# Performance work log

Measured on AMD Instinct MI355X. Metric: run time of the kernel, lower is better.

The kernel has to match this reference:

```python
import jax, jax.numpy as jnp
import numpy as np

MASK_SCORE = -1.0e15
LOG_2PI = float(np.log(2.0 * np.pi))


def setup_inputs() -> dict:
    key = jax.random.key(0)
    k1, k2, k3, k4 = jax.random.split(key, 4)
    B, H, N, T = 32, 256, 512, 2048
    encoder_outputs = jax.random.normal(k1, (B, H, N), dtype=jnp.float32)
    # positive integer-like durations in [1, 7]
    durations = jnp.round(jax.random.uniform(k2, (B, N), minval=1.0, maxval=7.0)).astype(jnp.float32)
    # well-conditioned variances
    vars_ = jax.random.uniform(k3, (B, N), minval=0.5, maxval=2.0, dtype=jnp.float32)
    input_lengths = jax.random.randint(k4, (B,), N // 2, N + 1, dtype=jnp.int32)
    return {"encoder_outputs": encoder_outputs, "durations": durations,
            "vars": vars_, "input_lengths": input_lengths, "T": T}


def reference(encoder_outputs, durations, vars, input_lengths, T):
    # encoder_outputs: [B, H, N] -> [B, N, H]
    x = jnp.swapaxes(encoder_outputs, 1, 2)
    B, N, H = x.shape
    # Gaussian centers: cumsum(d) - d/2  -> [B, N]
    c = jnp.cumsum(durations, axis=1) - 0.5 * durations
    t = jnp.arange(T, dtype=x.dtype)  # [T]
    v = vars[:, :, None]              # [B, N, 1]
    # Gaussian log-density scores: [B, N, T]
    w_t = -0.5 * (LOG_2PI + jnp.log(v) + jnp.square(t[None, None, :] - c[:, :, None]) / v)
    # mask invalid phoneme positions (index >= length) along N
    invalid = jnp.arange(N)[None, :] >= input_lengths[:, None]  # [B, N]
    w_t = jnp.where(invalid[:, :, None], MASK_SCORE, w_t)
    # softmax over phoneme axis N, then weighted sum of encoder states
    w_t = jax.nn.softmax(w_t, axis=1)                 # [B, N, T]
    out = jnp.einsum('bnt,bnh->bth', w_t, x)          # [B, T, H]
    return jnp.swapaxes(out, 1, 2)                    # [B, H, T]
```

## Files before the change

### kernel.cpp

```cpp
#include <hip/hip_runtime.h>
#include <math.h>
#include <stdint.h>

static constexpr int B = 32, H = 256, N = 512, T = 2048;
static constexpr int TTILE = 64;
static constexpr int KC = 64;
static constexpr float kLOG_2PI = 1.8378770664093453f;
static constexpr float kLOG2E   = 1.4426950408889634f;
static constexpr float kNEG_BIG = -3.0e38f;
static constexpr float kRANGE_DELTA = 26.0f;

typedef __attribute__((ext_vector_type(8))) short bf16x8;
typedef __attribute__((ext_vector_type(4))) float f32x4;

static __device__ __forceinline__ short f2bf(float f) {
  unsigned u = __float_as_uint(f);
  unsigned r = (u + 0x7fffu + ((u >> 16) & 1u)) >> 16;
  return (short)r;
}

__global__ void k_prep(const float* __restrict__ dur, const float* __restrict__ vars,
                       const int* __restrict__ lens,
                       float4* __restrict__ psg, float2* __restrict__ bstat) {
  const int b = blockIdx.x;
  const int lane = threadIdx.x;
  const int L = lens[b];
  float running = 0.f;
  float rc[N / 64], ra2[N / 64], rq2[N / 64];
  float a2max = kNEG_BIG, a2min = -kNEG_BIG, q2min = -kNEG_BIG, q2max = kNEG_BIG;
  float dmax = 0.f, clast = 0.f;
#pragma unroll
  for (int i = 0; i < N / 64; ++i) {
    const int n = i * 64 + lane;
    const float d = dur[b * N + n];
    float x = d;
#pragma unroll
    for (int off = 1; off < 64; off <<= 1) {
      float up = __shfl_up(x, off, 64);
      if (lane >= off) x += up;
    }
    const float cc = running + x - 0.5f * d;
    running += __shfl(x, 63, 64);
    const float v = vars[b * N + n];
    const float a2v = -0.5f * (kLOG_2PI + logf(v)) * kLOG2E;
    const float q2v = 0.5f * kLOG2E / v;
    rc[i] = cc; ra2[i] = a2v; rq2[i] = q2v;
    if (n < L) {
      a2max = fmaxf(a2max, a2v); a2min = fminf(a2min, a2v);
      q2min = fminf(q2min, q2v); q2max = fmaxf(q2max, q2v);
      dmax = fmaxf(dmax, d);
      if (n == L - 1) clast = cc;
    }
  }
#pragma unroll
  for (int off = 32; off; off >>= 1) {
    a2max = fmaxf(a2max, __shfl_xor(a2max, off, 64));
    a2min = fminf(a2min, __shfl_xor(a2min, off, 64));
    q2min = fminf(q2min, __shfl_xor(q2min, off, 64));
    q2max = fmaxf(q2max, __shfl_xor(q2max, off, 64));
    dmax  = fmaxf(dmax,  __shfl_xor(dmax,  off, 64));
    clast = fmaxf(clast, __shfl_xor(clast, off, 64));
  }
  const float dnb = 0.5f * dmax;
  const float m_lower = a2min - q2max * dnb * dnb;
  const float thr = m_lower - kRANGE_DELTA;
#pragma unroll
  for (int i = 0; i < N / 64; ++i) {
    const int n = i * 64 + lane;
    const float rr = sqrtf(fmaxf(ra2[i] - thr, 0.f) / rq2[i]);
    psg[(size_t)b * N + n] = make_float4(rc[i], ra2[i], rq2[i], rr);
  }
  if (lane == 0) bstat[b] = make_float2(a2max, clast);
}

__global__ __launch_bounds__(256) void k_fused(
    const float* __restrict__ enc, const float4* __restrict__ psg,
    const int* __restrict__ lens, const float2* __restrict__ bstat,
    float* __restrict__ out) {
  __shared__ float4 ps[N];
  __shared__ float m_lds[TTILE];
  __shared__ int range_sh[2];

  const int b = blockIdx.y;
  const int t0 = blockIdx.x * TTILE;
  const int tid = threadIdx.x;
  const int lane = tid & 63;
  const int wave = tid >> 6;
  const int L = lens[b];
  const float2 bs = bstat[b];
  const float* encb = enc + (size_t)b * H * N;
  const float4* psb = psg + (size_t)b * N;

  const int l15 = lane & 15;
  const int lhi = lane >> 4;
  const int arow0 = wave * 64 + l15;

  const bool tile_near = ((float)(t0 + TTILE - 1) <= bs.y);
  int nlo, nhi;
  float mt[4];

  if (tile_near) {
    const float tmin = (float)t0, tmax = (float)(t0 + TTILE - 1);
    int lo = N, hi = -1;
#pragma unroll
    for (int rr = 0; rr < 8; ++rr) {
      const int n = rr * 64 + lane;
      const float4 p4 = psb[n];
      if (n < L && (p4.x - p4.w) <= tmax && (p4.x + p4.w) >= tmin) {
        lo = min(lo, n); hi = max(hi, n);
      }
    }
#pragma unroll
    for (int off = 32; off; off >>= 1) {
      lo = min(lo, __shfl_xor(lo, off, 64));
      hi = max(hi, __shfl_xor(hi, off, 64));
    }
    nlo = lo; nhi = hi;
#pragma unroll
    for (int tt = 0; tt < 4; ++tt) mt[tt] = bs.x;
  } else {
    if (tid == 0) { range_sh[0] = N; range_sh[1] = -1; }
    for (int i = tid; i < N; i += 256) ps[i] = psb[i];
    __syncthreads();
    const int tl = tid >> 2, j = tid & 3;
    const float tf = (float)(t0 + tl);
    const int iL = (L + 3) >> 2;
    float mA = kNEG_BIG, mB = kNEG_BIG;
    int i1 = 0;
    for (; i1 + 1 < iL; i1 += 2) {
      const int n1 = i1 * 4 + j, n2 = n1 + 4;
      const float4 p1 = ps[n1];
      const float tc1 = tf - p1.x;
      const float w1 = fmaf(-p1.z, tc1 * tc1, p1.y);
      mA = fmaxf(mA, (n1 < L) ? w1 : kNEG_BIG);
      const float4 p2 = ps[n2];
      const float tc2 = tf - p2.x;
      const float w2 = fmaf(-p2.z, tc2 * tc2, p2.y);
      mB = fmaxf(mB, (n2 < L) ? w2 : kNEG_BIG);
    }
    if (i1 < iL) {
      const int n1 = i1 * 4 + j;
      const float4 p1 = ps[n1];
      const float tc1 = tf - p1.x;
      const float w1 = fmaf(-p1.z, tc1 * tc1, p1.y);
      mA = fmaxf(mA, (n1 < L) ? w1 : kNEG_BIG);
    }
    float m = fmaxf(mA, mB);
    m = fmaxf(m, __shfl_xor(m, 1, 64));
    m = fmaxf(m, __shfl_xor(m, 2, 64));
    if (j == 0) m_lds[tl] = m;

    const float thr = m - kRANGE_DELTA;
    int lo = N, hi = -1;
    for (int i2 = 0; i2 < iL; ++i2) {
      const int n = i2 * 4 + j;
      const float4 p4 = ps[n];
      const float tc = tf - p4.x;
      const float ww = fmaf(-p4.z, tc * tc, p4.y);
      if (n < L && ww >= thr) { lo = min(lo, n); hi = max(hi, n); }
    }
#pragma unroll
    for (int off = 32; off; off >>= 1) {
      lo = min(lo, __shfl_xor(lo, off, 64));
      hi = max(hi, __shfl_xor(hi, off, 64));
    }
    if (lane == 0) { atomicMin(&range_sh[0], lo); atomicMax(&range_sh[1], hi); }
    __syncthreads();
    nlo = range_sh[0]; nhi = range_sh[1];
#pragma unroll
    for (int tt = 0; tt < 4; ++tt) mt[tt] = m_lds[tt * 16 + l15];
  }

  if (nhi < 0) { nlo = 0; nhi = L - 1; }
  nlo = max(0, min(nlo, N - 1)); nhi = max(nlo, min(nhi, N - 1));

  f32x4 acc[4][4];
#pragma unroll
  for (int mf = 0; mf < 4; ++mf)
#pragma unroll
    for (int tt = 0; tt < 4; ++tt) acc[mf][tt] = (f32x4){0.f, 0.f, 0.f, 0.f};
  float psum[4] = {0.f, 0.f, 0.f, 0.f};

  int wb = nlo & ~3;
  while (true) {
    const int wbc = min(wb, N - KC);
    const int wlo = max(wb, nlo);
#pragma unroll
    for (int kk = 0; kk < KC; kk += 32) {
      const int colk = wbc + kk;
      if (colk > nhi || colk + 31 < wlo) continue;
      const int col = colk + lhi * 8;
      float4 pq[8];
#pragma unroll
      for (int jj = 0; jj < 8; ++jj) pq[jj] = psb[col + jj];
      bf16x8 aF[4];
#pragma unroll
      for (int mf = 0; mf < 4; ++mf) {
        const float* src = encb + (size_t)(arow0 + mf * 16) * N + col;
        const float4 v0 = *(const float4*)(src);
        const float4 v1 = *(const float4*)(src + 4);
        aF[mf][0] = f2bf(v0.x); aF[mf][1] = f2bf(v0.y);
        aF[mf][2] = f2bf(v0.z); aF[mf][3] = f2bf(v0.w);
        aF[mf][4] = f2bf(v1.x); aF[mf][5] = f2bf(v1.y);
        aF[mf][6] = f2bf(v1.z); aF[mf][7] = f2bf(v1.w);
      }
#pragma unroll
      for (int tt = 0; tt < 4; ++tt) {
        const float tft = (float)(t0 + tt * 16 + l15);
        const float mtt = mt[tt];
        bf16x8 bF;
        float psv = 0.f;
#pragma unroll
        for (int jj = 0; jj < 8; ++jj) {
          const int n = col + jj;
          const float tc = tft - pq[jj].x;
          const float w2v = fmaf(-pq[jj].z, tc * tc, pq[jj].y);
          const float pv = (n >= wlo && n <= nhi) ? exp2f(w2v - mtt) : 0.f;
          psv += pv;
          bF[jj] = f2bf(pv);
        }
        psum[tt] += psv;
#pragma unroll
        for (int mf = 0; mf < 4; ++mf)
          acc[mf][tt] = __builtin_amdgcn_mfma_f32_16x16x32_bf16(aF[mf], bF, acc[mf][tt], 0, 0, 0);
      }
    }
    if (wbc + KC > nhi) break;
    wb = wbc + KC;
  }

#pragma unroll
  for (int tt = 0; tt < 4; ++tt) {
    float s = psum[tt];
    s += __shfl_xor(s, 16, 64);
    s += __shfl_xor(s, 32, 64);
    const float is = 1.0f / s;
    const int t = tt * 16 + l15;
#pragma unroll
    for (int mf = 0; mf < 4; ++mf) {
      const int h = wave * 64 + mf * 16 + lhi * 4;
#pragma unroll
      for (int r = 0; r < 4; ++r) {
        out[((size_t)(b * H + h + r)) * T + t0 + t] = acc[mf][tt][r] * is;
      }
    }
  }
}

extern "C" void kernel_launch(void* const* d_in, const int* in_sizes, int n_in,
                              void* d_out, int out_size, void* d_ws, size_t ws_size,
                              hipStream_t stream) {
  const float* enc  = (const float*)d_in[0];
  const float* dur  = (const float*)d_in[1];
  const float* vars = (const float*)d_in[2];
  const int*   lens = (const int*)d_in[3];
  float* out = (float*)d_out;

  char* ws = (char*)d_ws;
  float4* psg   = (float4*)ws;
  float2* bstat = (float2*)(psg + B * N);

  k_prep<<<B, 64, 0, stream>>>(dur, vars, lens, psg, bstat);
  k_fused<<<dim3(T / TTILE, B), 256, 0, stream>>>(enc, psg, lens, bstat, out);
}
```

Measured before the change: 41.38 us.

## Split near/far tiles into separate kernels and bound far-tile scan range

Splits the fused kernel into a near-tile kernel, which uses a constant per-batch max, and a far-tile kernel, which narrows its max and range scan to phonemes whose centres could still matter. The far path no longer stages the parameters in shared memory and starts scanning from a lower bound computed in prep. It also halves the K chunk to 32 and switches to the library bf16 conversion. The intent is less divergent code per kernel and less scanning work for far tiles, at the cost of one extra launch and many early-exiting blocks.

```diff
diff --git a/kernel.cpp b/kernel.cpp
--- a/kernel.cpp
+++ b/kernel.cpp
@@ -1,10 +1,11 @@
 #include <hip/hip_runtime.h>
+#include <hip/hip_bf16.h>
 #include <math.h>
 #include <stdint.h>
 
 static constexpr int B = 32, H = 256, N = 512, T = 2048;
 static constexpr int TTILE = 64;
-static constexpr int KC = 64;
+static constexpr int KC = 32;
 static constexpr float kLOG_2PI = 1.8378770664093453f;
 static constexpr float kLOG2E   = 1.4426950408889634f;
 static constexpr float kNEG_BIG = -3.0e38f;
@@ -14,14 +15,13 @@
 typedef __attribute__((ext_vector_type(4))) float f32x4;
 
 static __device__ __forceinline__ short f2bf(float f) {
-  unsigned u = __float_as_uint(f);
-  unsigned r = (u + 0x7fffu + ((u >> 16) & 1u)) >> 16;
-  return (short)r;
+  __hip_bfloat16 h = __float2bfloat16(f);
+  return *reinterpret_cast<short*>(&h);
 }
 
 __global__ void k_prep(const float* __restrict__ dur, const float* __restrict__ vars,
                        const int* __restrict__ lens,
-                       float4* __restrict__ psg, float2* __restrict__ bstat) {
+                       float4* __restrict__ psg, float4* __restrict__ bstat) {
   const int b = blockIdx.x;
   const int lane = threadIdx.x;
   const int L = lens[b];
@@ -70,109 +70,49 @@
     const float rr = sqrtf(fmaxf(ra2[i] - thr, 0.f) / rq2[i]);
     psg[(size_t)b * N + n] = make_float4(rc[i], ra2[i], rq2[i], rr);
   }
-  if (lane == 0) bstat[b] = make_float2(a2max, clast);
-}
-
-__global__ __launch_bounds__(256) void k_fused(
+  if (lane == 0) {
+    bstat[b] = make_float4(a2max, clast,
+                           sqrtf(q2max / q2min) - 1.0f,
+                           sqrtf(fmaxf(a2max - a2min + kRANGE_DELTA + 1.0f, 0.f) / q2min));
+  }
+}
+
+__global__ __launch_bounds__(256) void k_near(
     const float* __restrict__ enc, const float4* __restrict__ psg,
-    const int* __restrict__ lens, const float2* __restrict__ bstat,
+    const int* __restrict__ lens, const float4* __restrict__ bstat,
     float* __restrict__ out) {
-  __shared__ float4 ps[N];
-  __shared__ float m_lds[TTILE];
-  __shared__ int range_sh[2];
-
   const int b = blockIdx.y;
   const int t0 = blockIdx.x * TTILE;
+  const float4 bs = bstat[b];
+  if ((float)(t0 + TTILE - 1) > bs.y) return;
   const int tid = threadIdx.x;
   const int lane = tid & 63;
   const int wave = tid >> 6;
   const int L = lens[b];
-  const float2 bs = bstat[b];
   const float* encb = enc + (size_t)b * H * N;
   const float4* psb = psg + (size_t)b * N;
-
-  const int l15 = lane & 15;
-  const int lhi = lane >> 4;
+  const int l15 = lane & 15, lhi = lane >> 4;
   const int arow0 = wave * 64 + l15;
 
-  const bool tile_near = ((float)(t0 + TTILE - 1) <= bs.y);
-  int nlo, nhi;
-  float mt[4];
-
-  if (tile_near) {
-    const float tmin = (float)t0, tmax = (float)(t0 + TTILE - 1);
-    int lo = N, hi = -1;
-#pragma unroll
-    for (int rr = 0; rr < 8; ++rr) {
-      const int n = rr * 64 + lane;
-      const float4 p4 = psb[n];
-      if (n < L && (p4.x - p4.w) <= tmax && (p4.x + p4.w) >= tmin) {
-        lo = min(lo, n); hi = max(hi, n);
-      }
-    }
-#pragma unroll
-    for (int off = 32; off; off >>= 1) {
-      lo = min(lo, __shfl_xor(lo, off, 64));
-      hi = max(hi, __shfl_xor(hi, off, 64));
-    }
-    nlo = lo; nhi = hi;
-#pragma unroll
-    for (int tt = 0; tt < 4; ++tt) mt[tt] = bs.x;
-  } else {
-    if (tid == 0) { range_sh[0] = N; range_sh[1] = -1; }
-    for (int i = tid; i < N; i += 256) ps[i] = psb[i];
-    __syncthreads();
-    const int tl = tid >> 2, j = tid & 3;
-    const float tf = (float)(t0 + tl);
-    const int iL = (L + 3) >> 2;
-    float mA = kNEG_BIG, mB = kNEG_BIG;
-    int i1 = 0;
-    for (; i1 + 1 < iL; i1 += 2) {
-      const int n1 = i1 * 4 + j, n2 = n1 + 4;
-      const float4 p1 = ps[n1];
-      const float tc1 = tf - p1.x;
-      const float w1 = fmaf(-p1.z, tc1 * tc1, p1.y);
-      mA = fmaxf(mA, (n1 < L) ? w1 : kNEG_BIG);
-      const float4 p2 = ps[n2];
-      const float tc2 = tf - p2.x;
-      const float w2 = fmaf(-p2.z, tc2 * tc2, p2.y);
-      mB = fmaxf(mB, (n2 < L) ? w2 : kNEG_BIG);
-    }
-    if (i1 < iL) {
-      const int n1 = i1 * 4 + j;
-      const float4 p1 = ps[n1];
-      const float tc1 = tf - p1.x;
-      const float w1 = fmaf(-p1.z, tc1 * tc1, p1.y);
-      mA = fmaxf(mA, (n1 < L) ? w1 : kNEG_BIG);
-    }
-    float m = fmaxf(mA, mB);
-    m = fmaxf(m, __shfl_xor(m, 1, 64));
-    m = fmaxf(m, __shfl_xor(m, 2, 64));
-    if (j == 0) m_lds[tl] = m;
-
-    const float thr = m - kRANGE_DELTA;
-    int lo = N, hi = -1;
-    for (int i2 = 0; i2 < iL; ++i2) {
-      const int n = i2 * 4 + j;
-      const float4 p4 = ps[n];
-      const float tc = tf - p4.x;
-      const float ww = fmaf(-p4.z, tc * tc, p4.y);
-      if (n < L && ww >= thr) { lo = min(lo, n); hi = max(hi, n); }
-    }
-#pragma unroll
-    for (int off = 32; off; off >>= 1) {
-      lo = min(lo, __shfl_xor(lo, off, 64));
-      hi = max(hi, __shfl_xor(hi, off, 64));
-    }
-    if (lane == 0) { atomicMin(&range_sh[0], lo); atomicMax(&range_sh[1], hi); }
-    __syncthreads();
-    nlo = range_sh[0]; nhi = range_sh[1];
-#pragma unroll
-    for (int tt = 0; tt < 4; ++tt) mt[tt] = m_lds[tt * 16 + l15];
-  }
-
-  if (nhi < 0) { nlo = 0; nhi = L - 1; }
-  nlo = max(0, min(nlo, N - 1)); nhi = max(nlo, min(nhi, N - 1));
+  const float tmin = (float)t0, tmax = (float)(t0 + TTILE - 1);
+  int lo = N, hi = -1;
+#pragma unroll
+  for (int rr = 0; rr < 8; ++rr) {
+    const int n = rr * 64 + lane;
+    const float4 p4 = psb[n];
+    if (n < L && (p4.x - p4.w) <= tmax && (p4.x + p4.w) >= tmin) {
+      lo = min(lo, n); hi = max(hi, n);
+    }
+  }
+#pragma unroll
+  for (int off = 32; off; off >>= 1) {
+    lo = min(lo, __shfl_xor(lo, off, 64));
+    hi = max(hi, __shfl_xor(hi, off, 64));
+  }
+  if (hi < 0) { lo = 0; hi = L - 1; }
+  int nlo = max(0, min(lo, L - 1));
+  int nhi = max(nlo, min(hi, L - 1));
+  const float mconst = bs.x;
 
   f32x4 acc[4][4];
 #pragma unroll
@@ -185,45 +125,39 @@
   while (true) {
     const int wbc = min(wb, N - KC);
     const int wlo = max(wb, nlo);
-#pragma unroll
-    for (int kk = 0; kk < KC; kk += 32) {
-      const int colk = wbc + kk;
-      if (colk > nhi || colk + 31 < wlo) continue;
-      const int col = colk + lhi * 8;
-      float4 pq[8];
-#pragma unroll
-      for (int jj = 0; jj < 8; ++jj) pq[jj] = psb[col + jj];
-      bf16x8 aF[4];
-#pragma unroll
-      for (int mf = 0; mf < 4; ++mf) {
-        const float* src = encb + (size_t)(arow0 + mf * 16) * N + col;
-        const float4 v0 = *(const float4*)(src);
-        const float4 v1 = *(const float4*)(src + 4);
-        aF[mf][0] = f2bf(v0.x); aF[mf][1] = f2bf(v0.y);
-        aF[mf][2] = f2bf(v0.z); aF[mf][3] = f2bf(v0.w);
-        aF[mf][4] = f2bf(v1.x); aF[mf][5] = f2bf(v1.y);
-        aF[mf][6] = f2bf(v1.z); aF[mf][7] = f2bf(v1.w);
+    const int col = wbc + lhi * 8;
+    float4 pq[8];
+#pragma unroll
+    for (int jj = 0; jj < 8; ++jj) pq[jj] = psb[col + jj];
+    bf16x8 aF[4];
+#pragma unroll
+    for (int mf = 0; mf < 4; ++mf) {
+      const float* src = encb + (size_t)(arow0 + mf * 16) * N + col;
+      const float4 v0 = *(const float4*)(src);
+      const float4 v1 = *(const float4*)(src + 4);
+      aF[mf][0] = f2bf(v0.x); aF[mf][1] = f2bf(v0.y);
+      aF[mf][2] = f2bf(v0.z); aF[mf][3] = f2bf(v0.w);
+      aF[mf][4] = f2bf(v1.x); aF[mf][5] = f2bf(v1.y);
+      aF[mf][6] = f2bf(v1.z); aF[mf][7] = f2bf(v1.w);
+    }
+#pragma unroll
+    for (int tt = 0; tt < 4; ++tt) {
+      const float tft = (float)(t0 + tt * 16 + l15);
+      bf16x8 bF;
+      float psv = 0.f;
+#pragma unroll
+      for (int jj = 0; jj < 8; ++jj) {
+        const int n = col + jj;
+        const float tc = tft - pq[jj].x;
+        const float w2v = fmaf(-pq[jj].z, tc * tc, pq[jj].y);
+        const float pv = (n >= wlo && n <= nhi) ? exp2f(w2v - mconst) : 0.f;
+        psv += pv;
+        bF[jj] = f2bf(pv);
       }
-#pragma unroll
-      for (int tt = 0; tt < 4; ++tt) {
-        const float tft = (float)(t0 + tt * 16 + l15);
-        const float mtt = mt[tt];
-        bf16x8 bF;
-        float psv = 0.f;
-#pragma unroll
-        for (int jj = 0; jj < 8; ++jj) {
-          const int n = col + jj;
-          const float tc = tft - pq[jj].x;
-          const float w2v = fmaf(-pq[jj].z, tc * tc, pq[jj].y);
-          const float pv = (n >= wlo && n <= nhi) ? exp2f(w2v - mtt) : 0.f;
-          psv += pv;
-          bF[jj] = f2bf(pv);
-        }
-        psum[tt] += psv;
-#pragma unroll
-        for (int mf = 0; mf < 4; ++mf)
-          acc[mf][tt] = __builtin_amdgcn_mfma_f32_16x16x32_bf16(aF[mf], bF, acc[mf][tt], 0, 0, 0);
-      }
+      psum[tt] += psv;
+#pragma unroll
+      for (int mf = 0; mf < 4; ++mf)
+        acc[mf][tt] = __builtin_amdgcn_mfma_f32_16x16x32_bf16(aF[mf], bF, acc[mf][tt], 0, 0, 0);
     }
     if (wbc + KC > nhi) break;
     wb = wbc + KC;
@@ -240,9 +174,161 @@
     for (int mf = 0; mf < 4; ++mf) {
       const int h = wave * 64 + mf * 16 + lhi * 4;
 #pragma unroll
-      for (int r = 0; r < 4; ++r) {
+      for (int r = 0; r < 4; ++r)
         out[((size_t)(b * H + h + r)) * T + t0 + t] = acc[mf][tt][r] * is;
+    }
+  }
+}
+
+__global__ __launch_bounds__(256) void k_far(
+    const float* __restrict__ enc, const float4* __restrict__ psg,
+    const int* __restrict__ lens, const float4* __restrict__ bstat,
+    float* __restrict__ out) {
+  __shared__ float m_lds[TTILE];
+  __shared__ int range_sh[2];
+
+  const int b = blockIdx.y;
+  const int t0 = blockIdx.x * TTILE;
+  const float4 bs = bstat[b];
+  if ((float)(t0 + TTILE - 1) <= bs.y) return;
+  const int tid = threadIdx.x;
+  const int lane = tid & 63;
+  const int wave = tid >> 6;
+  const int L = lens[b];
+  const float* encb = enc + (size_t)b * H * N;
+  const float4* psb = psg + (size_t)b * N;
+  const int l15 = lane & 15, lhi = lane >> 4;
+  const int arow0 = wave * 64 + l15;
+
+  if (tid == 0) { range_sh[0] = N; range_sh[1] = -1; }
+  __syncthreads();
+
+  const float tmin = (float)t0, tmax = (float)(t0 + TTILE - 1);
+  const float cmin_far = bs.y - bs.z * (tmax - bs.y) - bs.w;
+
+  int wlo_n = N;
+#pragma unroll
+  for (int rr = 0; rr < 8; ++rr) {
+    const int n = rr * 64 + lane;
+    const float4 p4 = psb[n];
+    const bool hit = (n < L) &&
+        ((p4.x >= cmin_far) ||
+         ((p4.x - p4.w) <= tmax && (p4.x + p4.w) >= tmin));
+    if (hit) wlo_n = min(wlo_n, n);
+  }
+#pragma unroll
+  for (int off = 32; off; off >>= 1) wlo_n = min(wlo_n, __shfl_xor(wlo_n, off, 64));
+  const int n_lo = min(wlo_n, L - 1);
+
+  const int tl = tid >> 2, j = tid & 3;
+  const float tf = (float)(t0 + tl);
+  float mA = kNEG_BIG, mB = kNEG_BIG;
+  int nn = n_lo + j;
+  for (; nn + 4 < L; nn += 8) {
+    const float4 p1 = psb[nn];
+    const float tc1 = tf - p1.x;
+    mA = fmaxf(mA, fmaf(-p1.z, tc1 * tc1, p1.y));
+    const float4 p2 = psb[nn + 4];
+    const float tc2 = tf - p2.x;
+    mB = fmaxf(mB, fmaf(-p2.z, tc2 * tc2, p2.y));
+  }
+  if (nn < L) {
+    const float4 p1 = psb[nn];
+    const float tc1 = tf - p1.x;
+    mA = fmaxf(mA, fmaf(-p1.z, tc1 * tc1, p1.y));
+  }
+  float m = fmaxf(mA, mB);
+  m = fmaxf(m, __shfl_xor(m, 1, 64));
+  m = fmaxf(m, __shfl_xor(m, 2, 64));
+  if (j == 0) m_lds[tl] = m;
+
+  const float thr = m - kRANGE_DELTA;
+  int lo = N, hi = -1;
+  for (int n2 = n_lo + j; n2 < L; n2 += 4) {
+    const float4 p4 = psb[n2];
+    const float tc = tf - p4.x;
+    const float ww = fmaf(-p4.z, tc * tc, p4.y);
+    if (ww >= thr) { lo = min(lo, n2); hi = max(hi, n2); }
+  }
+#pragma unroll
+  for (int off = 32; off; off >>= 1) {
+    lo = min(lo, __shfl_xor(lo, off, 64));
+    hi = max(hi, __shfl_xor(hi, off, 64));
+  }
+  if (lane == 0) { atomicMin(&range_sh[0], lo); atomicMax(&range_sh[1], hi); }
+  __syncthreads();
+
+  int nlo = range_sh[0], nhi = range_sh[1];
+  if (nhi < 0) { nlo = n_lo; nhi = L - 1; }
+  nlo = max(0, min(nlo, L - 1));
+  nhi = max(nlo, min(nhi, L - 1));
+  float mt[4];
+#pragma unroll
+  for (int tt = 0; tt < 4; ++tt) mt[tt] = m_lds[tt * 16 + l15];
+
+  f32x4 acc[4][4];
+#pragma unroll
+  for (int mf = 0; mf < 4; ++mf)
+#pragma unroll
+    for (int tt = 0; tt < 4; ++tt) acc[mf][tt] = (f32x4){0.f, 0.f, 0.f, 0.f};
+  float psum[4] = {0.f, 0.f, 0.f, 0.f};
+
+  int wb = nlo & ~3;
+  while (true) {
+    const int wbc = min(wb, N - KC);
+    const int wlo = max(wb, nlo);
+    const int col = wbc + lhi * 8;
+    float4 pq[8];
+#pragma unroll
+    for (int jj = 0; jj < 8; ++jj) pq[jj] = psb[col + jj];
+    bf16x8 aF[4];
+#pragma unroll
+    for (int mf = 0; mf < 4; ++mf) {
+      const float* src = encb + (size_t)(arow0 + mf * 16) * N + col;
+      const float4 v0 = *(const float4*)(src);
+      const float4 v1 = *(const float4*)(src + 4);
+      aF[mf][0] = f2bf(v0.x); aF[mf][1] = f2bf(v0.y);
+      aF[mf][2] = f2bf(v0.z); aF[mf][3] = f2bf(v0.w);
+      aF[mf][4] = f2bf(v1.x); aF[mf][5] = f2bf(v1.y);
+      aF[mf][6] = f2bf(v1.z); aF[mf][7] = f2bf(v1.w);
+    }
+#pragma unroll
+    for (int tt = 0; tt < 4; ++tt) {
+      const float tft = (float)(t0 + tt * 16 + l15);
+      const float mtt = mt[tt];
+      bf16x8 bF;
+      float psv = 0.f;
+#pragma unroll
+      for (int jj = 0; jj < 8; ++jj) {
+        const int n = col + jj;
+        const float tc = tft - pq[jj].x;
+        const float w2v = fmaf(-pq[jj].z, tc * tc, pq[jj].y);
+        const float pv = (n >= wlo && n <= nhi) ? exp2f(w2v - mtt) : 0.f;
+        psv += pv;
+        bF[jj] = f2bf(pv);
       }
+      psum[tt] += psv;
+#pragma unroll
+      for (int mf = 0; mf < 4; ++mf)
+        acc[mf][tt] = __builtin_amdgcn_mfma_f32_16x16x32_bf16(aF[mf], bF, acc[mf][tt], 0, 0, 0);
+    }
+    if (wbc + KC > nhi) break;
+    wb = wbc + KC;
+  }
+
+#pragma unroll
+  for (int tt = 0; tt < 4; ++tt) {
+    float s = psum[tt];
+    s += __shfl_xor(s, 16, 64);
+    s += __shfl_xor(s, 32, 64);
+    const float is = 1.0f / s;
+    const int t = tt * 16 + l15;
+#pragma unroll
+    for (int mf = 0; mf < 4; ++mf) {
+      const int h = wave * 64 + mf * 16 + lhi * 4;
+#pragma unroll
+      for (int r = 0; r < 4; ++r)
+        out[((size_t)(b * H + h + r)) * T + t0 + t] = acc[mf][tt][r] * is;
     }
   }
 }
@@ -258,8 +344,9 @@
 
   char* ws = (char*)d_ws;
   float4* psg   = (float4*)ws;
-  float2* bstat = (float2*)(psg + B * N);
+  float4* bstat = (float4*)(psg + B * N);
 
   k_prep<<<B, 64, 0, stream>>>(dur, vars, lens, psg, bstat);
-  k_fused<<<dim3(T / TTILE, B), 256, 0, stream>>>(enc, psg, lens, bstat, out);
-}
+  k_near<<<dim3(T / TTILE, B), 256, 0, stream>>>(enc, psg, lens, bstat, out);
+  k_far<<<dim3(T / TTILE, B), 256, 0, stream>>>(enc, psg, lens, bstat, out);
+}
```

New measurement: 62.86 us. 51.9% more time.

## Halve time tile, drop LDS staging of phoneme params, use bf16 intrinsic

Applied to the files above, without the earlier changes.

Cuts the time tile from 64 to 32. This doubles the grid and narrows each tile's phoneme range, at the cost of less reuse of the encoder loads across time. The far-tile max and range scan now read phoneme parameters straight from global/L2 instead of staging them in LDS, with 8 threads per time step instead of 4. The hand-written float-to-bf16 rounding is replaced with the HIP __float2bfloat16 intrinsic.

```diff
diff --git a/kernel.cpp b/kernel.cpp
--- a/kernel.cpp
+++ b/kernel.cpp
@@ -1,10 +1,12 @@
 #include <hip/hip_runtime.h>
+#include <hip/hip_bf16.h>
 #include <math.h>
 #include <stdint.h>
 
 static constexpr int B = 32, H = 256, N = 512, T = 2048;
-static constexpr int TTILE = 64;
+static constexpr int TTILE = 32;
 static constexpr int KC = 64;
+static constexpr int NTT = TTILE / 16;
 static constexpr float kLOG_2PI = 1.8378770664093453f;
 static constexpr float kLOG2E   = 1.4426950408889634f;
 static constexpr float kNEG_BIG = -3.0e38f;
@@ -14,9 +16,8 @@
 typedef __attribute__((ext_vector_type(4))) float f32x4;
 
 static __device__ __forceinline__ short f2bf(float f) {
-  unsigned u = __float_as_uint(f);
-  unsigned r = (u + 0x7fffu + ((u >> 16) & 1u)) >> 16;
-  return (short)r;
+  __hip_bfloat16 h = __float2bfloat16(f);
+  return *reinterpret_cast<short*>(&h);
 }
 
 __global__ void k_prep(const float* __restrict__ dur, const float* __restrict__ vars,
@@ -77,7 +78,6 @@
     const float* __restrict__ enc, const float4* __restrict__ psg,
     const int* __restrict__ lens, const float2* __restrict__ bstat,
     float* __restrict__ out) {
-  __shared__ float4 ps[N];
   __shared__ float m_lds[TTILE];
   __shared__ int range_sh[2];
 
@@ -97,7 +97,7 @@
 
   const bool tile_near = ((float)(t0 + TTILE - 1) <= bs.y);
   int nlo, nhi;
-  float mt[4];
+  float mt[NTT];
 
   if (tile_near) {
     const float tmin = (float)t0, tmax = (float)(t0 + TTILE - 1);
@@ -117,30 +117,29 @@
     }
     nlo = lo; nhi = hi;
 #pragma unroll
-    for (int tt = 0; tt < 4; ++tt) mt[tt] = bs.x;
+    for (int tt = 0; tt < NTT; ++tt) mt[tt] = bs.x;
   } else {
     if (tid == 0) { range_sh[0] = N; range_sh[1] = -1; }
-    for (int i = tid; i < N; i += 256) ps[i] = psb[i];
     __syncthreads();
-    const int tl = tid >> 2, j = tid & 3;
+    const int tl = tid >> 3, j = tid & 7;
     const float tf = (float)(t0 + tl);
-    const int iL = (L + 3) >> 2;
+    const int iL = (L + 7) >> 3;
     float mA = kNEG_BIG, mB = kNEG_BIG;
     int i1 = 0;
     for (; i1 + 1 < iL; i1 += 2) {
-      const int n1 = i1 * 4 + j, n2 = n1 + 4;
-      const float4 p1 = ps[n1];
+      const int n1 = i1 * 8 + j, n2 = n1 + 8;
+      const float4 p1 = psb[n1];
       const float tc1 = tf - p1.x;
       const float w1 = fmaf(-p1.z, tc1 * tc1, p1.y);
       mA = fmaxf(mA, (n1 < L) ? w1 : kNEG_BIG);
-      const float4 p2 = ps[n2];
+      const float4 p2 = psb[n2];
       const float tc2 = tf - p2.x;
       const float w2 = fmaf(-p2.z, tc2 * tc2, p2.y);
       mB = fmaxf(mB, (n2 < L) ? w2 : kNEG_BIG);
     }
     if (i1 < iL) {
-      const int n1 = i1 * 4 + j;
-      const float4 p1 = ps[n1];
+      const int n1 = i1 * 8 + j;
+      const float4 p1 = psb[n1];
       const float tc1 = tf - p1.x;
       const float w1 = fmaf(-p1.z, tc1 * tc1, p1.y);
       mA = fmaxf(mA, (n1 < L) ? w1 : kNEG_BIG);
@@ -148,13 +147,14 @@
     float m = fmaxf(mA, mB);
     m = fmaxf(m, __shfl_xor(m, 1, 64));
     m = fmaxf(m, __shfl_xor(m, 2, 64));
+    m = fmaxf(m, __shfl_xor(m, 4, 64));
     if (j == 0) m_lds[tl] = m;
 
     const float thr = m - kRANGE_DELTA;
     int lo = N, hi = -1;
     for (int i2 = 0; i2 < iL; ++i2) {
-      const int n = i2 * 4 + j;
-      const float4 p4 = ps[n];
+      const int n = i2 * 8 + j;
+      const float4 p4 = psb[n];
       const float tc = tf - p4.x;
       const float ww = fmaf(-p4.z, tc * tc, p4.y);
       if (n < L && ww >= thr) { lo = min(lo, n); hi = max(hi, n); }
@@ -168,18 +168,20 @@
     __syncthreads();
     nlo = range_sh[0]; nhi = range_sh[1];
 #pragma unroll
-    for (int tt = 0; tt < 4; ++tt) mt[tt] = m_lds[tt * 16 + l15];
+    for (int tt = 0; tt < NTT; ++tt) mt[tt] = m_lds[tt * 16 + l15];
   }
 
   if (nhi < 0) { nlo = 0; nhi = L - 1; }
   nlo = max(0, min(nlo, N - 1)); nhi = max(nlo, min(nhi, N - 1));
 
-  f32x4 acc[4][4];
+  f32x4 acc[4][NTT];
 #pragma unroll
   for (int mf = 0; mf < 4; ++mf)
 #pragma unroll
-    for (int tt = 0; tt < 4; ++tt) acc[mf][tt] = (f32x4){0.f, 0.f, 0.f, 0.f};
-  float psum[4] = {0.f, 0.f, 0.f, 0.f};
+    for (int tt = 0; tt < NTT; ++tt) acc[mf][tt] = (f32x4){0.f, 0.f, 0.f, 0.f};
+  float psum[NTT];
+#pragma unroll
+  for (int tt = 0; tt < NTT; ++tt) psum[tt] = 0.f;
 
   int wb = nlo & ~3;
   while (true) {
@@ -205,7 +207,7 @@
         aF[mf][6] = f2bf(v1.z); aF[mf][7] = f2bf(v1.w);
       }
 #pragma unroll
-      for (int tt = 0; tt < 4; ++tt) {
+      for (int tt = 0; tt < NTT; ++tt) {
         const float tft = (float)(t0 + tt * 16 + l15);
         const float mtt = mt[tt];
         bf16x8 bF;
@@ -230,7 +232,7 @@
   }
 
 #pragma unroll
-  for (int tt = 0; tt < 4; ++tt) {
+  for (int tt = 0; tt < NTT; ++tt) {
     float s = psum[tt];
     s += __shfl_xor(s, 16, 64);
     s += __shfl_xor(s, 32, 64);
```

After: 57.89 us. 1.4x slower.
